# Kernel tuning notes

Measured on AMD Instinct MI355X. Metric: run time of the kernel, lower is better.

Reference implementation:

```python
import jax, jax.numpy as jnp
import numpy as np

NEG_SLOPE = 0.2

def gatv2_conv(x, src, dst, Wl, Wr, att, b, num_nodes):
    # GATv2: e = att . leaky_relu(Wl x_src + Wr x_dst); segment softmax over dst; scatter-add of alpha * Wl x_src
    xl = x @ Wl  # [N, out]
    xr = x @ Wr  # [N, out]
    m = xl[src] + xr[dst]                        # [E, out] edge gather
    e = jax.nn.leaky_relu(m, NEG_SLOPE) @ att    # [E]
    emax = jax.ops.segment_max(e, dst, num_segments=num_nodes)
    ee = jnp.exp(e - emax[dst])
    denom = jax.ops.segment_sum(ee, dst, num_segments=num_nodes)
    alpha = ee / denom[dst]                      # [E]
    out = jax.ops.segment_sum(alpha[:, None] * xl[src], dst, num_segments=num_nodes)
    return out + b

def setup_inputs() -> dict:
    key = jax.random.key(0)
    ks = jax.random.split(key, 24)
    N, E, F, H, B = 40000, 640000, 128, 128, 64
    inp = {
        'x': jax.random.normal(ks[0], (N, F), dtype=jnp.float32),
        'edge_index': jax.random.randint(ks[1], (2, E), 0, N),
        'batch': jnp.sort(jax.random.randint(ks[2], (N,), 0, B)),
        'day': jax.random.randint(ks[3], (B,), 0, 7),
        'hour': jax.random.randint(ks[4], (B,), 0, 24),
    }
    def glorot(k, shape):
        lim = float(np.sqrt(6.0 / (shape[0] + shape[1])))
        return jax.random.uniform(k, shape, jnp.float32, -lim, lim)
    # GATv2 layers (heads=1)
    inp['Wl1'] = glorot(ks[5], (F, H)); inp['Wr1'] = glorot(ks[6], (F, H))
    inp['att1'] = glorot(ks[7], (H, 1))[:, 0]; inp['b1'] = jnp.zeros((H,), jnp.float32)
    inp['Wl2'] = glorot(ks[8], (H, H)); inp['Wr2'] = glorot(ks[9], (H, H))
    inp['att2'] = glorot(ks[10], (H, 1))[:, 0]; inp['b2'] = jnp.zeros((H,), jnp.float32)
    inp['Wl3'] = glorot(ks[11], (H, H)); inp['Wr3'] = glorot(ks[12], (H, H))
    inp['att3'] = glorot(ks[13], (H, 1))[:, 0]; inp['b3'] = jnp.zeros((H,), jnp.float32)
    # embeddings
    inp['day_tab'] = jax.random.normal(ks[14], (7, 64), dtype=jnp.float32)
    inp['hour_tab'] = jax.random.normal(ks[15], (24, 64), dtype=jnp.float32)
    # MLP head (weights stored [in, out])
    inp['W1'] = glorot(ks[16], (256, 256)); inp['bl1'] = jnp.zeros((256,), jnp.float32)
    inp['W2'] = glorot(ks[17], (256, 256)); inp['bl2'] = jnp.zeros((256,), jnp.float32)
    inp['W3'] = glorot(ks[18], (256, 1));   inp['bl3'] = jnp.zeros((1,), jnp.float32)
    return inp

def reference(x, edge_index, batch, day, hour,
              Wl1, Wr1, att1, b1, Wl2, Wr2, att2, b2, Wl3, Wr3, att3, b3,
              day_tab, hour_tab, W1, bl1, W2, bl2, W3, bl3):
    N = x.shape[0]
    B = day.shape[0]
    # add self loops (PyG default add_self_loops=True)
    loops = jnp.arange(N)
    src = jnp.concatenate([edge_index[0], loops])
    dst = jnp.concatenate([edge_index[1], loops])
    h = gatv2_conv(x, src, dst, Wl1, Wr1, att1, b1, N)
    h = jax.nn.relu(h)
    h = gatv2_conv(h, src, dst, Wl2, Wr2, att2, b2, N)
    h = jax.nn.relu(h)
    h = gatv2_conv(h, src, dst, Wl3, Wr3, att3, b3, N)
    # global mean pool over graphs
    sums = jax.ops.segment_sum(h, batch, num_segments=B)
    cnts = jax.ops.segment_sum(jnp.ones((N,), h.dtype), batch, num_segments=B)
    pooled = sums / jnp.maximum(cnts, 1.0)[:, None]      # [B, 128]
    feats = jnp.concatenate([pooled, day_tab[day], hour_tab[hour]], axis=1)  # [B, 256]
    z = jax.nn.relu(feats @ W1 + bl1)
    z = jax.nn.relu(z @ W2 + bl2)
    return z @ W3 + bl3  # [B, 1]
```

## Files before the change

### kernel.cpp

```cpp
#include <hip/hip_runtime.h>
#include <math.h>

#define NEG_SLOPE 0.2f
#define POOL_CHUNKS 8

typedef __attribute__((ext_vector_type(8))) short bf16x8;
typedef __attribute__((ext_vector_type(4))) float f32x4;

__device__ __forceinline__ void split_bf16(float x, short& hi, short& lo) {
    unsigned u = __float_as_uint(x);
    unsigned uh = u & 0xFFFF0000u;
    float r = x - __uint_as_float(uh);
    hi = (short)(uh >> 16);
    lo = (short)(__float_as_uint(r) >> 16);
}

__device__ __forceinline__ unsigned f2bf_rne(float x) {
    unsigned u = __float_as_uint(x);
    return (u + 0x7fffu + ((u >> 16) & 1u)) >> 16;
}

__global__ __launch_bounds__(256, 1) void node_gemm(
    const float* __restrict__ h, const float* __restrict__ Wl,
    const float* __restrict__ Wr, unsigned* __restrict__ xlb,
    float* __restrict__ xr, int N, int nTiles)
{
    const int w   = threadIdx.x >> 6;
    const int l   = threadIdx.x & 63;
    const int l15 = l & 15, lg = l >> 4;

    const float* __restrict__ Wsel = (w < 2) ? Wl : Wr;
    const int cbase = (w & 1) * 64;

    bf16x8 bh[4][4], bl_[4][4];
    #pragma unroll
    for (int ct = 0; ct < 4; ++ct) {
        const int c = cbase + ct * 16 + l15;
        #pragma unroll
        for (int kt = 0; kt < 4; ++kt) {
            #pragma unroll
            for (int i = 0; i < 8; ++i) {
                float v = Wsel[(kt * 32 + lg * 8 + i) * 128 + c];
                short hi, lo; split_bf16(v, hi, lo);
                bh[ct][kt][i] = hi; bl_[ct][kt][i] = lo;
            }
        }
    }

    for (int tile = blockIdx.x; tile < nTiles; tile += gridDim.x) {
        const int row0 = tile * 64;

        f32x4 acc[4][4];
        #pragma unroll
        for (int rt = 0; rt < 4; ++rt)
            #pragma unroll
            for (int ct = 0; ct < 4; ++ct)
                acc[rt][ct] = (f32x4){0.f, 0.f, 0.f, 0.f};

        #pragma unroll
        for (int rt = 0; rt < 4; ++rt) {
            int row = row0 + rt * 16 + l15;
            int rowc = row < N ? row : N - 1;
            bf16x8 ah[4], al[4];
            #pragma unroll
            for (int kt = 0; kt < 4; ++kt) {
                const float4 v0 = *(const float4*)&h[(size_t)rowc * 128 + kt * 32 + lg * 8];
                const float4 v1 = *(const float4*)&h[(size_t)rowc * 128 + kt * 32 + lg * 8 + 4];
                const float vv[8] = {v0.x, v0.y, v0.z, v0.w, v1.x, v1.y, v1.z, v1.w};
                #pragma unroll
                for (int i = 0; i < 8; ++i) {
                    short hi, lo; split_bf16(vv[i], hi, lo);
                    ah[kt][i] = hi; al[kt][i] = lo;
                }
            }
            #pragma unroll
            for (int kt = 0; kt < 4; ++kt) {
                #pragma unroll
                for (int ct = 0; ct < 4; ++ct) {
                    acc[rt][ct] = __builtin_amdgcn_mfma_f32_16x16x32_bf16(
                        ah[kt], bh[ct][kt], acc[rt][ct], 0, 0, 0);
                    acc[rt][ct] = __builtin_amdgcn_mfma_f32_16x16x32_bf16(
                        al[kt], bh[ct][kt], acc[rt][ct], 0, 0, 0);
                    acc[rt][ct] = __builtin_amdgcn_mfma_f32_16x16x32_bf16(
                        ah[kt], bl_[ct][kt], acc[rt][ct], 0, 0, 0);
                }
            }
        }

        if (w < 2) {
            #pragma unroll
            for (int rt = 0; rt < 4; ++rt) {
                #pragma unroll
                for (int ct = 0; ct < 4; ++ct) {
                    #pragma unroll
                    for (int j = 0; j < 4; ++j) {
                        int row = row0 + rt * 16 + lg * 4 + j;
                        unsigned o = f2bf_rne(acc[rt][ct][j]);
                        unsigned pr = (unsigned)__shfl_xor((int)o, 1);
                        if (!(l15 & 1) && row < N) {
                            int cp = (cbase + ct * 16 + l15) >> 1;
                            xlb[(size_t)row * 64 + cp] = o | (pr << 16);
                        }
                    }
                }
            }
        } else {
            #pragma unroll
            for (int rt = 0; rt < 4; ++rt) {
                #pragma unroll
                for (int ct = 0; ct < 4; ++ct) {
                    #pragma unroll
                    for (int j = 0; j < 4; ++j) {
                        int row = row0 + rt * 16 + lg * 4 + j;
                        if (row < N)
                            xr[(size_t)row * 128 + cbase + ct * 16 + l15] = acc[rt][ct][j];
                    }
                }
            }
        }
    }
}

__global__ __launch_bounds__(256) void edge_hist(
    const int* __restrict__ ei, int* __restrict__ deg, int E, int ET)
{
    int eid = blockIdx.x * blockDim.x + threadIdx.x;
    if (eid >= ET) return;
    int dst = (eid < E) ? ei[E + eid] : eid - E;
    atomicAdd(&deg[dst], 1);
}

__global__ __launch_bounds__(256) void scan_block(
    const int* __restrict__ in, int* __restrict__ out_excl,
    int* __restrict__ bsum, int N)
{
    __shared__ int sm[256];
    int t = threadIdx.x, i = blockIdx.x * 256 + t;
    int v = (i < N) ? in[i] : 0;
    sm[t] = v;
    __syncthreads();
    int x = v;
    for (int o = 1; o < 256; o <<= 1) {
        int u = (t >= o) ? sm[t - o] : 0;
        __syncthreads();
        x += u; sm[t] = x;
        __syncthreads();
    }
    if (i < N) out_excl[i] = x - v;
    if (t == 255) bsum[blockIdx.x] = x;
}

__global__ __launch_bounds__(256) void scan_sums(int* __restrict__ bsum, int nb)
{
    __shared__ int sm[256];
    int t = threadIdx.x;
    int v = (t < nb) ? bsum[t] : 0;
    sm[t] = v;
    __syncthreads();
    int x = v;
    for (int o = 1; o < 256; o <<= 1) {
        int u = (t >= o) ? sm[t - o] : 0;
        __syncthreads();
        x += u; sm[t] = x;
        __syncthreads();
    }
    if (t < nb) bsum[t] = x - v;
}

__global__ __launch_bounds__(256) void scan_final(
    const int* __restrict__ excl, const int* __restrict__ bsum,
    int* __restrict__ rowptr, int N, int ET)
{
    int i = blockIdx.x * blockDim.x + threadIdx.x;
    if (i > N) return;
    rowptr[i] = (i < N) ? (excl[i] + bsum[i >> 8]) : ET;
}

__global__ __launch_bounds__(256) void edge_fill(
    const int* __restrict__ ei, const int* __restrict__ rowptr,
    int* __restrict__ cursor, int* __restrict__ srcs, int E, int ET)
{
    int eid = blockIdx.x * blockDim.x + threadIdx.x;
    if (eid >= ET) return;
    int src, dst;
    if (eid < E) { src = ei[eid]; dst = ei[E + eid]; }
    else { src = dst = eid - E; }
    int pos = rowptr[dst] + atomicAdd(&cursor[dst], 1);
    srcs[pos] = src;
}

__global__ __launch_bounds__(256) void gatv2_aggregate(
    const unsigned* __restrict__ xlb, const float* __restrict__ xr,
    const int* __restrict__ rowptr, const int* __restrict__ srcs,
    const float* __restrict__ att, const float* __restrict__ b,
    float* __restrict__ hout, int N, int do_relu)
{
    int n = blockIdx.x * 4 + (threadIdx.x >> 6);
    if (n >= N) return;
    const int lane = threadIdx.x & 63;
    const int hl = lane & 15;
    const int g  = lane >> 4;

    float xr8[8], at8[8];
    {
        const float4 a0 = *(const float4*)&xr[(size_t)n * 128 + hl * 8];
        const float4 a1 = *(const float4*)&xr[(size_t)n * 128 + hl * 8 + 4];
        xr8[0]=a0.x; xr8[1]=a0.y; xr8[2]=a0.z; xr8[3]=a0.w;
        xr8[4]=a1.x; xr8[5]=a1.y; xr8[6]=a1.z; xr8[7]=a1.w;
        const float4 t0 = *(const float4*)&att[hl * 8];
        const float4 t1 = *(const float4*)&att[hl * 8 + 4];
        at8[0]=t0.x; at8[1]=t0.y; at8[2]=t0.z; at8[3]=t0.w;
        at8[4]=t1.x; at8[5]=t1.y; at8[6]=t1.z; at8[7]=t1.w;
    }

    int r0 = rowptr[n], r1 = rowptr[n + 1];
    float m = -INFINITY, s = 0.f;
    float acc[8];
    #pragma unroll
    for (int c = 0; c < 8; ++c) acc[c] = 0.f;

    auto unpack = [&](const uint4 q, float* vv) {
        unsigned u;
        u = q.x; vv[0] = __uint_as_float(u << 16); vv[1] = __uint_as_float(u & 0xFFFF0000u);
        u = q.y; vv[2] = __uint_as_float(u << 16); vv[3] = __uint_as_float(u & 0xFFFF0000u);
        u = q.z; vv[4] = __uint_as_float(u << 16); vv[5] = __uint_as_float(u & 0xFFFF0000u);
        u = q.w; vv[6] = __uint_as_float(u << 16); vv[7] = __uint_as_float(u & 0xFFFF0000u);
    };
    auto score = [&](const float* vv) -> float {
        float p = 0.f;
        #pragma unroll
        for (int c = 0; c < 8; ++c) {
            float t = vv[c] + xr8[c];
            t = fmaxf(t, NEG_SLOPE * t);
            p += t * at8[c];
        }
        return p;
    };
    auto online = [&](float p, const float* vv) {
        if (p > m + 15.f) {
            float f = __expf(m - p);
            s *= f;
            #pragma unroll
            for (int c = 0; c < 8; ++c) acc[c] *= f;
            m = p;
        }
        float w = __expf(p - m);
        s += w;
        #pragma unroll
        for (int c = 0; c < 8; ++c) acc[c] += w * vv[c];
    };

    int j = r0 + g;
    for (; j + 4 < r1; j += 8) {
        int sa = srcs[j], sb = srcs[j + 4];
        const uint4 qa = *(const uint4*)&xlb[(size_t)sa * 64 + hl * 4];
        const uint4 qb = *(const uint4*)&xlb[(size_t)sb * 64 + hl * 4];
        float va[8], vb[8];
        unpack(qa, va); unpack(qb, vb);
        float pa = score(va), pb = score(vb);
        #pragma unroll
        for (int off = 1; off < 16; off <<= 1) {
            pa += __shfl_xor(pa, off);
            pb += __shfl_xor(pb, off);
        }
        online(pa, va);
        online(pb, vb);
    }
    if (j < r1) {
        int sa = srcs[j];
        const uint4 qa = *(const uint4*)&xlb[(size_t)sa * 64 + hl * 4];
        float va[8];
        unpack(qa, va);
        float pa = score(va);
        #pragma unroll
        for (int off = 1; off < 16; off <<= 1) pa += __shfl_xor(pa, off);
        online(pa, va);
    }

    float mm = m;
    mm = fmaxf(mm, __shfl_xor(mm, 16));
    mm = fmaxf(mm, __shfl_xor(mm, 32));
    float f = __expf(m - mm);
    s *= f;
    #pragma unroll
    for (int c = 0; c < 8; ++c) acc[c] *= f;
    s += __shfl_xor(s, 16); s += __shfl_xor(s, 32);
    #pragma unroll
    for (int c = 0; c < 8; ++c) {
        acc[c] += __shfl_xor(acc[c], 16);
        acc[c] += __shfl_xor(acc[c], 32);
    }

    if (g == 0) {
        float inv = 1.f / s;
        float o[8];
        #pragma unroll
        for (int c = 0; c < 8; ++c) {
            o[c] = acc[c] * inv + b[hl * 8 + c];
            if (do_relu) o[c] = fmaxf(o[c], 0.f);
        }
        *(float4*)&hout[(size_t)n * 128 + hl * 8]     = make_float4(o[0], o[1], o[2], o[3]);
        *(float4*)&hout[(size_t)n * 128 + hl * 8 + 4] = make_float4(o[4], o[5], o[6], o[7]);
    }
}

__global__ __launch_bounds__(256) void graph_bounds(
    const int* __restrict__ batch, int* __restrict__ gstart, int N, int B)
{
    int b = blockIdx.x * blockDim.x + threadIdx.x;
    if (b > B) return;
    int lo = 0, hi = N;
    while (lo < hi) {
        int mid = (lo + hi) >> 1;
        if (batch[mid] < b) lo = mid + 1; else hi = mid;
    }
    gstart[b] = lo;
}

__global__ __launch_bounds__(256) void pool_graph(
    const float* __restrict__ h, const int* __restrict__ gstart,
    float* __restrict__ pooled)
{
    __shared__ float sm[128];
    const int b = blockIdx.x / POOL_CHUNKS;
    const int chunk = blockIdx.x % POOL_CHUNKS;
    const int t = threadIdx.x;
    const int col = t & 127, hf = t >> 7;
    const int r0 = gstart[b], r1 = gstart[b + 1];
    const int len = r1 - r0;
    const int c0 = r0 + (int)(((long long)len * chunk) / POOL_CHUNKS);
    const int c1 = r0 + (int)(((long long)len * (chunk + 1)) / POOL_CHUNKS);
    float s = 0.f;
    for (int r = c0 + hf; r < c1; r += 2)
        s += h[(size_t)r * 128 + col];
    if (hf) sm[col] = s;
    __syncthreads();
    if (!hf) atomicAdd(&pooled[b * 128 + col], s + sm[col]);
}

__global__ __launch_bounds__(256) void mlp_head(
    const float* __restrict__ pooled, const int* __restrict__ gstart,
    const int* __restrict__ day, const int* __restrict__ hour,
    const float* __restrict__ day_tab, const float* __restrict__ hour_tab,
    const float* __restrict__ W1, const float* __restrict__ bl1,
    const float* __restrict__ W2, const float* __restrict__ bl2,
    const float* __restrict__ W3, const float* __restrict__ bl3,
    float* __restrict__ out)
{
    __shared__ float f0[256], f1[256];
    const int b = blockIdx.x, t = threadIdx.x;
    float c = fmaxf((float)(gstart[b + 1] - gstart[b]), 1.f);
    if (t < 128)      f0[t] = pooled[b * 128 + t] / c;
    else if (t < 192) f0[t] = day_tab[day[b] * 64 + (t - 128)];
    else              f0[t] = hour_tab[hour[b] * 64 + (t - 192)];
    __syncthreads();
    float a = bl1[t];
    for (int k = 0; k < 256; ++k) a += f0[k] * W1[k * 256 + t];
    f1[t] = a > 0.f ? a : 0.f;
    __syncthreads();
    a = bl2[t];
    for (int k = 0; k < 256; ++k) a += f1[k] * W2[k * 256 + t];
    __syncthreads();
    f0[t] = a > 0.f ? a : 0.f;
    __syncthreads();
    f1[t] = f0[t] * W3[t];
    __syncthreads();
    for (int s2 = 128; s2 > 0; s2 >>= 1) {
        if (t < s2) f1[t] += f1[t + s2];
        __syncthreads();
    }
    if (t == 0) out[b] = f1[0] + bl3[0];
}

extern "C" void kernel_launch(void* const* d_in, const int* in_sizes, int n_in,
                              void* d_out, int out_size, void* d_ws, size_t ws_size,
                              hipStream_t stream) {
    const float* x        = (const float*)d_in[0];
    const int*   ei       = (const int*)d_in[1];
    const int*   batch    = (const int*)d_in[2];
    const int*   day      = (const int*)d_in[3];
    const int*   hour     = (const int*)d_in[4];
    const float* Wl[3]  = { (const float*)d_in[5],  (const float*)d_in[9],  (const float*)d_in[13] };
    const float* Wr[3]  = { (const float*)d_in[6],  (const float*)d_in[10], (const float*)d_in[14] };
    const float* att[3] = { (const float*)d_in[7],  (const float*)d_in[11], (const float*)d_in[15] };
    const float* bb[3]  = { (const float*)d_in[8],  (const float*)d_in[12], (const float*)d_in[16] };
    const float* day_tab  = (const float*)d_in[17];
    const float* hour_tab = (const float*)d_in[18];
    const float* W1 = (const float*)d_in[19]; const float* bl1 = (const float*)d_in[20];
    const float* W2 = (const float*)d_in[21]; const float* bl2 = (const float*)d_in[22];
    const float* W3 = (const float*)d_in[23]; const float* bl3 = (const float*)d_in[24];
    float* out = (float*)d_out;

    const int N  = in_sizes[0] / 128;
    const int E  = in_sizes[1] / 2;
    const int B  = in_sizes[3];
    const int ET = E + N;

    char* ws = (char*)d_ws;
    size_t off = 0;
    auto alloc = [&](size_t bytes) -> void* {
        void* p = ws + off;
        off += (bytes + 255) & ~(size_t)255;
        return p;
    };
    const size_t NB = (size_t)N * 128 * sizeof(float);
    unsigned* xlb = (unsigned*)alloc((size_t)N * 64 * sizeof(unsigned));
    float* xr     = (float*)alloc(NB);
    float* hbuf   = (float*)alloc(NB);
    int*   deg    = (int*)alloc((size_t)N * sizeof(int));
    int*   excl   = (int*)alloc((size_t)N * sizeof(int));
    int*   bsum   = (int*)alloc(256 * sizeof(int));
    int*   rowptr = (int*)alloc((size_t)(N + 1) * sizeof(int));
    int*   cursor = (int*)alloc((size_t)N * sizeof(int));
    int*   srcs   = (int*)alloc((size_t)ET * sizeof(int));
    int*   gstart = (int*)alloc((size_t)(B + 1) * sizeof(int));
    float* pooled = (float*)alloc((size_t)B * 128 * sizeof(float));
    (void)ws_size;

    const int nb = (N + 255) / 256;
    const int edge_grid  = (ET + 255) / 256;
    const int node_grid4 = (N + 3) / 4;
    const int nTiles     = (N + 63) / 64;
    const int gemm_grid  = (nTiles + 1) / 2;

    hipMemsetAsync(deg, 0, (size_t)N * sizeof(int), stream);
    hipMemsetAsync(cursor, 0, (size_t)N * sizeof(int), stream);
    edge_hist<<<edge_grid, 256, 0, stream>>>(ei, deg, E, ET);
    scan_block<<<nb, 256, 0, stream>>>(deg, excl, bsum, N);
    scan_sums<<<1, 256, 0, stream>>>(bsum, nb);
    scan_final<<<(N + 256) / 256, 256, 0, stream>>>(excl, bsum, rowptr, N, ET);
    edge_fill<<<edge_grid, 256, 0, stream>>>(ei, rowptr, cursor, srcs, E, ET);

    const float* hin = x;
    for (int l = 0; l < 3; ++l) {
        node_gemm<<<gemm_grid, 256, 0, stream>>>(hin, Wl[l], Wr[l], xlb, xr, N, nTiles);
        gatv2_aggregate<<<node_grid4, 256, 0, stream>>>(
            xlb, xr, rowptr, srcs, att[l], bb[l], hbuf, N, l < 2 ? 1 : 0);
        hin = hbuf;
    }

    graph_bounds<<<1, 256, 0, stream>>>(batch, gstart, N, B);
    hipMemsetAsync(pooled, 0, (size_t)B * 128 * sizeof(float), stream);
    pool_graph<<<B * POOL_CHUNKS, 256, 0, stream>>>(hbuf, gstart, pooled);
    mlp_head<<<B, 256, 0, stream>>>(pooled, gstart, day, hour, day_tab, hour_tab,
                                    W1, bl1, W2, bl2, W3, bl3, out);
}
```

Before: 326.1 us.

## Grid-stride GATv2 aggregate with 4-edge unrolled batched online softmax

Turns the aggregation kernel into a grid-stride loop over node quads with a capped grid of 2560 blocks. The attention vector is loaded once per block. The edge loop now handles four gathered neighbours per group per iteration, combining their weights with a single batched max-rescale instead of a branchy per-edge update. This raises memory-level parallelism on the bf16 gathers and cuts per-edge exp and rescale overhead. In exchange it uses more registers, always rescales the accumulator, and loses the one-node-per-wave launch scheduling.

```diff
diff --git a/kernel.cpp b/kernel.cpp
--- a/kernel.cpp
+++ b/kernel.cpp
@@ -193,114 +193,133 @@
     const unsigned* __restrict__ xlb, const float* __restrict__ xr,
     const int* __restrict__ rowptr, const int* __restrict__ srcs,
     const float* __restrict__ att, const float* __restrict__ b,
-    float* __restrict__ hout, int N, int do_relu)
-{
-    int n = blockIdx.x * 4 + (threadIdx.x >> 6);
-    if (n >= N) return;
+    float* __restrict__ hout, int N, int do_relu, int nQuads)
+{
     const int lane = threadIdx.x & 63;
+    const int wv = threadIdx.x >> 6;
     const int hl = lane & 15;
     const int g  = lane >> 4;
 
-    float xr8[8], at8[8];
+    float at8[8];
     {
-        const float4 a0 = *(const float4*)&xr[(size_t)n * 128 + hl * 8];
-        const float4 a1 = *(const float4*)&xr[(size_t)n * 128 + hl * 8 + 4];
-        xr8[0]=a0.x; xr8[1]=a0.y; xr8[2]=a0.z; xr8[3]=a0.w;
-        xr8[4]=a1.x; xr8[5]=a1.y; xr8[6]=a1.z; xr8[7]=a1.w;
         const float4 t0 = *(const float4*)&att[hl * 8];
         const float4 t1 = *(const float4*)&att[hl * 8 + 4];
         at8[0]=t0.x; at8[1]=t0.y; at8[2]=t0.z; at8[3]=t0.w;
         at8[4]=t1.x; at8[5]=t1.y; at8[6]=t1.z; at8[7]=t1.w;
     }
 
-    int r0 = rowptr[n], r1 = rowptr[n + 1];
-    float m = -INFINITY, s = 0.f;
-    float acc[8];
-    #pragma unroll
-    for (int c = 0; c < 8; ++c) acc[c] = 0.f;
-
-    auto unpack = [&](const uint4 q, float* vv) {
-        unsigned u;
-        u = q.x; vv[0] = __uint_as_float(u << 16); vv[1] = __uint_as_float(u & 0xFFFF0000u);
-        u = q.y; vv[2] = __uint_as_float(u << 16); vv[3] = __uint_as_float(u & 0xFFFF0000u);
-        u = q.z; vv[4] = __uint_as_float(u << 16); vv[5] = __uint_as_float(u & 0xFFFF0000u);
-        u = q.w; vv[6] = __uint_as_float(u << 16); vv[7] = __uint_as_float(u & 0xFFFF0000u);
-    };
-    auto score = [&](const float* vv) -> float {
-        float p = 0.f;
+    for (int q = blockIdx.x; q < nQuads; q += gridDim.x) {
+        const int n = q * 4 + wv;
+        if (n >= N) continue;
+
+        float xr8[8];
+        {
+            const float4 a0 = *(const float4*)&xr[(size_t)n * 128 + hl * 8];
+            const float4 a1 = *(const float4*)&xr[(size_t)n * 128 + hl * 8 + 4];
+            xr8[0]=a0.x; xr8[1]=a0.y; xr8[2]=a0.z; xr8[3]=a0.w;
+            xr8[4]=a1.x; xr8[5]=a1.y; xr8[6]=a1.z; xr8[7]=a1.w;
+        }
+
+        int r0 = rowptr[n], r1 = rowptr[n + 1];
+        float m = -INFINITY, s = 0.f;
+        float acc[8];
+        #pragma unroll
+        for (int c = 0; c < 8; ++c) acc[c] = 0.f;
+
+        auto unpack = [&](const uint4 q4, float* vv) {
+            unsigned u;
+            u = q4.x; vv[0] = __uint_as_float(u << 16); vv[1] = __uint_as_float(u & 0xFFFF0000u);
+            u = q4.y; vv[2] = __uint_as_float(u << 16); vv[3] = __uint_as_float(u & 0xFFFF0000u);
+            u = q4.z; vv[4] = __uint_as_float(u << 16); vv[5] = __uint_as_float(u & 0xFFFF0000u);
+            u = q4.w; vv[6] = __uint_as_float(u << 16); vv[7] = __uint_as_float(u & 0xFFFF0000u);
+        };
+        auto score = [&](const float* vv) -> float {
+            float p = 0.f;
+            #pragma unroll
+            for (int c = 0; c < 8; ++c) {
+                float t = vv[c] + xr8[c];
+                t = fmaxf(t, NEG_SLOPE * t);
+                p += t * at8[c];
+            }
+            return p;
+        };
+        auto online1 = [&](float p, const float* vv) {
+            float mn = fmaxf(m, p);
+            float f = __expf(m - mn);
+            float w = __expf(p - mn);
+            s = s * f + w;
+            #pragma unroll
+            for (int c = 0; c < 8; ++c) acc[c] = acc[c] * f + w * vv[c];
+            m = mn;
+        };
+
+        int j = r0 + g;
+        for (; j + 12 < r1; j += 16) {
+            int sa = srcs[j], sb = srcs[j + 4], sc = srcs[j + 8], sd = srcs[j + 12];
+            const uint4 qa = *(const uint4*)&xlb[(size_t)sa * 64 + hl * 4];
+            const uint4 qb = *(const uint4*)&xlb[(size_t)sb * 64 + hl * 4];
+            const uint4 qc = *(const uint4*)&xlb[(size_t)sc * 64 + hl * 4];
+            const uint4 qd = *(const uint4*)&xlb[(size_t)sd * 64 + hl * 4];
+            float va[8], vb[8], vc[8], vd[8];
+            unpack(qa, va); unpack(qb, vb); unpack(qc, vc); unpack(qd, vd);
+            float p0 = score(va), p1 = score(vb), p2 = score(vc), p3 = score(vd);
+            #pragma unroll
+            for (int off = 1; off < 16; off <<= 1) {
+                p0 += __shfl_xor(p0, off);
+                p1 += __shfl_xor(p1, off);
+                p2 += __shfl_xor(p2, off);
+                p3 += __shfl_xor(p3, off);
+            }
+            float m4 = fmaxf(fmaxf(p0, p1), fmaxf(p2, p3));
+            float w0 = __expf(p0 - m4), w1 = __expf(p1 - m4);
+            float w2 = __expf(p2 - m4), w3 = __expf(p3 - m4);
+            float s4 = (w0 + w1) + (w2 + w3);
+            float mn = fmaxf(m, m4);
+            float f  = __expf(m - mn);
+            float gw = __expf(m4 - mn);
+            s = s * f + s4 * gw;
+            w0 *= gw; w1 *= gw; w2 *= gw; w3 *= gw;
+            #pragma unroll
+            for (int c = 0; c < 8; ++c)
+                acc[c] = acc[c] * f + w0 * va[c] + w1 * vb[c] + w2 * vc[c] + w3 * vd[c];
+            m = mn;
+        }
+        for (; j < r1; j += 4) {
+            int sa = srcs[j];
+            const uint4 qa = *(const uint4*)&xlb[(size_t)sa * 64 + hl * 4];
+            float va[8];
+            unpack(qa, va);
+            float pa = score(va);
+            #pragma unroll
+            for (int off = 1; off < 16; off <<= 1) pa += __shfl_xor(pa, off);
+            online1(pa, va);
+        }
+
+        float mm = m;
+        mm = fmaxf(mm, __shfl_xor(mm, 16));
+        mm = fmaxf(mm, __shfl_xor(mm, 32));
+        float f = __expf(m - mm);
+        s *= f;
+        #pragma unroll
+        for (int c = 0; c < 8; ++c) acc[c] *= f;
+        s += __shfl_xor(s, 16); s += __shfl_xor(s, 32);
         #pragma unroll
         for (int c = 0; c < 8; ++c) {
-            float t = vv[c] + xr8[c];
-            t = fmaxf(t, NEG_SLOPE * t);
-            p += t * at8[c];
-        }
-        return p;
-    };
-    auto online = [&](float p, const float* vv) {
-        if (p > m + 15.f) {
-            float f = __expf(m - p);
-            s *= f;
-            #pragma unroll
-            for (int c = 0; c < 8; ++c) acc[c] *= f;
-            m = p;
-        }
-        float w = __expf(p - m);
-        s += w;
-        #pragma unroll
-        for (int c = 0; c < 8; ++c) acc[c] += w * vv[c];
-    };
-
-    int j = r0 + g;
-    for (; j + 4 < r1; j += 8) {
-        int sa = srcs[j], sb = srcs[j + 4];
-        const uint4 qa = *(const uint4*)&xlb[(size_t)sa * 64 + hl * 4];
-        const uint4 qb = *(const uint4*)&xlb[(size_t)sb * 64 + hl * 4];
-        float va[8], vb[8];
-        unpack(qa, va); unpack(qb, vb);
-        float pa = score(va), pb = score(vb);
-        #pragma unroll
-        for (int off = 1; off < 16; off <<= 1) {
-            pa += __shfl_xor(pa, off);
-            pb += __shfl_xor(pb, off);
-        }
-        online(pa, va);
-        online(pb, vb);
-    }
-    if (j < r1) {
-        int sa = srcs[j];
-        const uint4 qa = *(const uint4*)&xlb[(size_t)sa * 64 + hl * 4];
-        float va[8];
-        unpack(qa, va);
-        float pa = score(va);
-        #pragma unroll
-        for (int off = 1; off < 16; off <<= 1) pa += __shfl_xor(pa, off);
-        online(pa, va);
-    }
-
-    float mm = m;
-    mm = fmaxf(mm, __shfl_xor(mm, 16));
-    mm = fmaxf(mm, __shfl_xor(mm, 32));
-    float f = __expf(m - mm);
-    s *= f;
-    #pragma unroll
-    for (int c = 0; c < 8; ++c) acc[c] *= f;
-    s += __shfl_xor(s, 16); s += __shfl_xor(s, 32);
-    #pragma unroll
-    for (int c = 0; c < 8; ++c) {
-        acc[c] += __shfl_xor(acc[c], 16);
-        acc[c] += __shfl_xor(acc[c], 32);
-    }
-
-    if (g == 0) {
-        float inv = 1.f / s;
-        float o[8];
-        #pragma unroll
-        for (int c = 0; c < 8; ++c) {
-            o[c] = acc[c] * inv + b[hl * 8 + c];
-            if (do_relu) o[c] = fmaxf(o[c], 0.f);
-        }
-        *(float4*)&hout[(size_t)n * 128 + hl * 8]     = make_float4(o[0], o[1], o[2], o[3]);
-        *(float4*)&hout[(size_t)n * 128 + hl * 8 + 4] = make_float4(o[4], o[5], o[6], o[7]);
+            acc[c] += __shfl_xor(acc[c], 16);
+            acc[c] += __shfl_xor(acc[c], 32);
+        }
+
+        if (g == 0) {
+            float inv = 1.f / s;
+            float o[8];
+            #pragma unroll
+            for (int c = 0; c < 8; ++c) {
+                o[c] = acc[c] * inv + b[hl * 8 + c];
+                if (do_relu) o[c] = fmaxf(o[c], 0.f);
+            }
+            *(float4*)&hout[(size_t)n * 128 + hl * 8]     = make_float4(o[0], o[1], o[2], o[3]);
+            *(float4*)&hout[(size_t)n * 128 + hl * 8 + 4] = make_float4(o[4], o[5], o[6], o[7]);
+        }
     }
 }
 
@@ -419,7 +438,8 @@
 
     const int nb = (N + 255) / 256;
     const int edge_grid  = (ET + 255) / 256;
-    const int node_grid4 = (N + 3) / 4;
+    const int nQuads     = (N + 3) / 4;
+    const int agg_grid   = nQuads < 2560 ? nQuads : 2560;
     const int nTiles     = (N + 63) / 64;
     const int gemm_grid  = (nTiles + 1) / 2;
 
@@ -434,8 +454,8 @@
     const float* hin = x;
     for (int l = 0; l < 3; ++l) {
         node_gemm<<<gemm_grid, 256, 0, stream>>>(hin, Wl[l], Wr[l], xlb, xr, N, nTiles);
-        gatv2_aggregate<<<node_grid4, 256, 0, stream>>>(
-            xlb, xr, rowptr, srcs, att[l], bb[l], hbuf, N, l < 2 ? 1 : 0);
+        gatv2_aggregate<<<agg_grid, 256, 0, stream>>>(
+            xlb, xr, rowptr, srcs, att[l], bb[l], hbuf, N, l < 2 ? 1 : 0, nQuads);
         hin = hbuf;
     }
 
```

New measurement: 351.8 us. +7.9%, slower.
